# Performance work log

Hardware: AMD Instinct MI355X
Metric: run time of the kernel (lower is better)

Reference implementation:

```python
import jax, jax.numpy as jnp
import numpy as np

HIDDEN = 1024
INTER = 2816
NUM_EXPERTS = 8
TOP_K = 2
NUM_TASK_EXPERTS = 4
NUM_GENERALISTS = 2
NUM_TASKS = 8
BSZ, SEQ = 4, 2048
NEG = -1e9


def setup_inputs() -> dict:
    key = jax.random.key(0)
    ks = jax.random.split(key, 8)
    s = 1.0 / np.sqrt(HIDDEN)
    si = 1.0 / np.sqrt(INTER)
    return {
        "hidden_states": jax.random.normal(ks[0], (BSZ, SEQ, HIDDEN), jnp.float32),
        "task_id": 3,
        "task_emb": jax.random.normal(ks[1], (NUM_TASKS, HIDDEN), jnp.float32) * 0.02,
        "task_router_w": jax.random.uniform(ks[2], (NUM_EXPERTS, HIDDEN), jnp.float32, -s, s),
        "gate_weight": jax.random.uniform(ks[3], (NUM_EXPERTS, HIDDEN), jnp.float32, -s, s),
        "gate_proj": jax.random.uniform(ks[4], (NUM_EXPERTS, INTER, HIDDEN), jnp.float32, -s, s),
        "up_proj": jax.random.uniform(ks[5], (NUM_EXPERTS, INTER, HIDDEN), jnp.float32, -s, s),
        "down_proj": jax.random.uniform(ks[6], (NUM_EXPERTS, HIDDEN, INTER), jnp.float32, -si, si),
    }


def reference(hidden_states, task_id, task_emb, task_router_w, gate_weight,
              gate_proj, up_proj, down_proj):
    bsz, seq, dim = hidden_states.shape
    E, K = NUM_EXPERTS, TOP_K

    # ---- task-level routing: pick active experts ----
    task_vec = task_emb[task_id]                         # [d]
    task_scores = task_router_w @ task_vec               # [E]
    _, task_idx = jax.lax.top_k(task_scores, NUM_TASK_EXPERTS)
    gen_idx = jnp.arange(E - NUM_GENERALISTS, E)
    active_mask = jnp.zeros((E,), bool).at[task_idx].set(True).at[gen_idx].set(True)

    # ---- token-level gating over active experts (masked full softmax == subset softmax) ----
    gate_input = (hidden_states + task_vec).reshape(-1, dim)      # [N, d]
    logits = gate_input @ gate_weight.T                            # [N, E]
    scores = jax.nn.softmax(jnp.where(active_mask, logits, NEG), axis=-1)
    topk_gates, topk_idx = jax.lax.top_k(scores, K)                # [N, K]
    topk_gates = topk_gates / (topk_gates.sum(-1, keepdims=True) + 1e-6)

    # per-token per-expert combine weight: [N, E]
    comb = (jax.nn.one_hot(topk_idx, E, dtype=topk_gates.dtype) * topk_gates[..., None]).sum(1)

    # ---- expert MLPs (SwiGLU), dense-per-expert then weighted combine ----
    tokens = hidden_states.reshape(-1, dim)                        # [N, d]
    y = jnp.zeros_like(tokens)
    for e in range(E):
        h = jax.nn.silu(tokens @ gate_proj[e].T) * (tokens @ up_proj[e].T)  # [N, I]
        y = y + comb[:, e:e + 1] * (h @ down_proj[e].T)
    return y.reshape(bsz, seq, dim)
```

## Files before the change

### kernel.cpp

```cpp
#include <hip/hip_runtime.h>

#define HIDDEN 1024
#define INTER 2816
#define NE 8
#define NTOK 8192
#define CPAD 32
#define MAXTILES 136

typedef _Float16 f16;
typedef f16 f16x8 __attribute__((ext_vector_type(8)));
typedef f16 f16x4v __attribute__((ext_vector_type(4)));
typedef float f32x4 __attribute__((ext_vector_type(4)));

typedef __attribute__((address_space(3))) void lds_void;
typedef __attribute__((address_space(1))) void glb_void;

__device__ __forceinline__ void gl_lds16(const void* g, void* l) {
  __builtin_amdgcn_global_load_lds((const glb_void*)g, (lds_void*)l, 16, 0, 0);
}

__device__ __forceinline__ f32x4 mfma16(f16x8 a, f16x8 b, f32x4 c) {
  return __builtin_amdgcn_mfma_f32_16x16x32_f16(a, b, c, 0, 0, 0);
}

__device__ __forceinline__ f16x8 cvt8(float4 a, float4 b) {
  f16x8 v;
  v[0] = (f16)a.x; v[1] = (f16)a.y; v[2] = (f16)a.z; v[3] = (f16)a.w;
  v[4] = (f16)b.x; v[5] = (f16)b.y; v[6] = (f16)b.z; v[7] = (f16)b.w;
  return v;
}

__global__ void k_route(const float* __restrict__ task_emb,
                        const int* __restrict__ task_id_p,
                        const float* __restrict__ trw,
                        int* __restrict__ mask, int* __restrict__ counts) {
  __shared__ float sc[NE];
  const int tid = threadIdx.x;
  counts[tid] = 0;
  const float* tv = task_emb + (size_t)task_id_p[0] * HIDDEN;
  const int e = tid >> 5, l = tid & 31;
  float p = 0.f;
  for (int k = l; k < HIDDEN; k += 32) p += trw[e * HIDDEN + k] * tv[k];
  for (int o = 16; o > 0; o >>= 1) p += __shfl_down(p, o, 32);
  if (l == 0) sc[e] = p;
  __syncthreads();
  if (tid == 0) {
    int m[NE];
    bool used[NE];
    for (int i = 0; i < NE; ++i) { m[i] = 0; used[i] = false; }
    for (int it = 0; it < 4; ++it) {
      float best = -1e30f; int bi = 0;
      for (int i = 0; i < NE; ++i)
        if (!used[i] && sc[i] > best) { best = sc[i]; bi = i; }
      used[bi] = true; m[bi] = 1;
    }
    m[NE - 2] = 1; m[NE - 1] = 1;
    for (int i = 0; i < NE; ++i) mask[i] = m[i];
  }
}

__global__ __launch_bounds__(256) void k_gate_wcvt(
    const float* __restrict__ x, const float* __restrict__ task_emb,
    const int* __restrict__ task_id_p, const float* __restrict__ gw,
    const int* __restrict__ mask, int* __restrict__ counts,
    int* __restrict__ tok_list, int* __restrict__ tk_e,
    int* __restrict__ tk_pos, float* __restrict__ tk_w,
    f16* __restrict__ X16,
    const float* __restrict__ Wg, const float* __restrict__ Wu,
    const float* __restrict__ Wd,
    f16* __restrict__ Wg16, f16* __restrict__ Wu16, f16* __restrict__ Wd16) {
  const int tid = threadIdx.x;
  if (blockIdx.x >= 256) {
    const int bid = blockIdx.x - 256;
    const int e = bid / (3 * 1408);
    const int rem = bid - e * (3 * 1408);
    const int sel = rem / 1408;
    const int xb = rem - sel * 1408;
    if (!mask[e]) return;
    const float* src = sel == 0 ? Wg : (sel == 1 ? Wu : Wd);
    f16* dst = sel == 0 ? Wg16 : (sel == 1 ? Wu16 : Wd16);
    const size_t i = (size_t)e * INTER * HIDDEN + ((size_t)xb * 256 + tid) * 8;
    const float4* s4 = (const float4*)(src + i);
    float4 a = s4[0], b = s4[1];
    *(f16x8*)(dst + i) = cvt8(a, b);
    return;
  }
  const int g = tid >> 3, l8 = tid & 7;
  const int t = blockIdx.x * 32 + g;
  const float4* tv4 = (const float4*)(task_emb + (size_t)task_id_p[0] * HIDDEN);
  const float4* xr4 = (const float4*)(x + (size_t)t * HIDDEN);
  const float4* gw4 = (const float4*)gw;

  float acc[NE];
#pragma unroll
  for (int e = 0; e < NE; ++e) acc[e] = 0.f;
#pragma unroll 4
  for (int it = 0; it < 32; ++it) {
    const int idx4 = it * 8 + l8;
    float4 xv = xr4[idx4];
    f16x4v h4;
    h4[0] = (f16)xv.x; h4[1] = (f16)xv.y; h4[2] = (f16)xv.z; h4[3] = (f16)xv.w;
    *(f16x4v*)(X16 + (size_t)t * HIDDEN + idx4 * 4) = h4;
    float4 tvv = tv4[idx4];
    const float gx = xv.x + tvv.x, gy = xv.y + tvv.y;
    const float gz = xv.z + tvv.z, gwv = xv.w + tvv.w;
#pragma unroll
    for (int e = 0; e < NE; ++e) {
      float4 w = gw4[e * 256 + idx4];
      acc[e] += gx * w.x + gy * w.y + gz * w.z + gwv * w.w;
    }
  }
#pragma unroll
  for (int e = 0; e < NE; ++e) {
    acc[e] += __shfl_down(acc[e], 4, 8);
    acc[e] += __shfl_down(acc[e], 2, 8);
    acc[e] += __shfl_down(acc[e], 1, 8);
  }

  __shared__ int s_e0[32], s_e1[32], s_r0[32], s_r1[32], s_base[NE];
  __shared__ float s_w0[32], s_w1[32];

  if (l8 == 0) {
    float mx = -1e30f;
    for (int e = 0; e < NE; ++e) if (mask[e] && acc[e] > mx) mx = acc[e];
    float pr[NE]; float s = 0.f;
    for (int e = 0; e < NE; ++e) {
      pr[e] = mask[e] ? expf(acc[e] - mx) : 0.f;
      s += pr[e];
    }
    int i0 = 0; float v0 = -1.f;
    for (int e = 0; e < NE; ++e) if (pr[e] > v0) { v0 = pr[e]; i0 = e; }
    int i1 = (i0 == 0) ? 1 : 0; float v1 = -1.f;
    for (int e = 0; e < NE; ++e) if (e != i0 && pr[e] > v1) { v1 = pr[e]; i1 = e; }
    float g0 = v0 / s, g1 = v1 / s;
    float d = g0 + g1 + 1e-6f;
    s_e0[g] = i0; s_e1[g] = i1;
    s_w0[g] = g0 / d; s_w1[g] = g1 / d;
  }
  __syncthreads();
  if (tid == 0) {
    int cnt[NE];
#pragma unroll
    for (int e = 0; e < NE; ++e) cnt[e] = 0;
    for (int i = 0; i < 32; ++i) {
      s_r0[i] = cnt[s_e0[i]]++;
      s_r1[i] = cnt[s_e1[i]]++;
    }
    for (int e = 0; e < NE; ++e)
      s_base[e] = cnt[e] ? atomicAdd(&counts[e * CPAD], cnt[e]) : 0;
  }
  __syncthreads();
  if (l8 == 0) {
    const int e0 = s_e0[g], e1 = s_e1[g];
    const int p0 = s_base[e0] + s_r0[g];
    const int p1 = s_base[e1] + s_r1[g];
    tok_list[e0 * NTOK + p0] = t;
    tok_list[e1 * NTOK + p1] = t;
    tk_e[t] = e0; tk_e[NTOK + t] = e1;
    tk_pos[t] = p0; tk_pos[NTOK + t] = p1;
    tk_w[t] = s_w0[g]; tk_w[NTOK + t] = s_w1[g];
  }
}

__global__ void k_tiles(const int* __restrict__ counts, int* __restrict__ tiles) {
  if (threadIdx.x != 0) return;
  int* te = tiles + 1;
  int* tm = te + MAXTILES;
  int* tp = tm + MAXTILES;
  int* tn = tp + MAXTILES;
  int p = 0, nt = 0;
  for (int e = 0; e < NE; ++e) {
    const int c = counts[e * CPAD];
    for (int m0 = 0; m0 < c; m0 += 128) {
      te[nt] = e; tm[nt] = m0; tp[nt] = p; tn[nt] = c; ++nt;
    }
    p += c;
  }
  tiles[0] = nt;
}

__global__ __launch_bounds__(256, 2) void k_gateup16(
    const f16* __restrict__ X16, const f16* __restrict__ Wg16,
    const f16* __restrict__ Wu16, const int* __restrict__ tiles,
    const int* __restrict__ tok_list, f16* __restrict__ H) {
  const int yt = blockIdx.y;
  if (yt >= tiles[0]) return;
  const int e = tiles[1 + yt];
  const int m0 = tiles[1 + MAXTILES + yt];
  const int pbase = tiles[1 + 2 * MAXTILES + yt];
  const int ne = tiles[1 + 3 * MAXTILES + yt];
  const int n0 = blockIdx.x * 64;

  __shared__ __align__(16) f16 As[128][64];
  __shared__ __align__(16) f16 Bg[64][64];
  __shared__ __align__(16) f16 Bu[64][64];
  __shared__ int toks[128];

  const int tid = threadIdx.x;
  if (tid < 128) {
    int r = m0 + tid;
    toks[tid] = tok_list[e * NTOK + (r < ne ? r : ne - 1)];
  }
  __syncthreads();

  const int row8 = tid >> 3;
  const int sw = ((tid & 7) ^ (row8 & 7)) * 8;
  const f16* asrc[4];
#pragma unroll
  for (int l = 0; l < 4; ++l)
    asrc[l] = X16 + (size_t)toks[l * 32 + row8] * HIDDEN + sw;
  f16* aldst0 = &As[0][0] + tid * 8;
  const size_t ewoff = (size_t)e * INTER * HIDDEN;
  const f16* gsrc0 = Wg16 + ewoff + (size_t)(n0 + row8) * HIDDEN + sw;
  const f16* usrc0 = Wu16 + ewoff + (size_t)(n0 + row8) * HIDDEN + sw;
  f16* gdst0 = &Bg[0][0] + tid * 8;
  f16* udst0 = &Bu[0][0] + tid * 8;

  const int lane = tid & 63;
  const int wave = tid >> 6;
  const int wm = (wave >> 1) * 64;
  const int wn = (wave & 1) * 32;
  const int l15 = lane & 15, grp = lane >> 4;

  const f32x4 zf = {0.f, 0.f, 0.f, 0.f};
  f32x4 accg[4][2], accu[4][2];
#pragma unroll
  for (int i = 0; i < 4; ++i)
#pragma unroll
    for (int j = 0; j < 2; ++j) { accg[i][j] = zf; accu[i][j] = zf; }

#pragma unroll 1
  for (int k0 = 0; k0 < HIDDEN; k0 += 64) {
#pragma unroll
    for (int l = 0; l < 4; ++l)
      gl_lds16(asrc[l] + k0, aldst0 + l * 2048);
    gl_lds16(gsrc0 + k0, gdst0);
    gl_lds16(gsrc0 + k0 + 32 * HIDDEN, gdst0 + 2048);
    gl_lds16(usrc0 + k0, udst0);
    gl_lds16(usrc0 + k0 + 32 * HIDDEN, udst0 + 2048);
    __syncthreads();

#pragma unroll
    for (int h = 0; h < 2; ++h) {
      const int pc = (((h * 4 + grp) ^ (l15 & 7)) << 4);
      f16x8 af[4];
#pragma unroll
      for (int i = 0; i < 4; ++i)
        af[i] = *(const f16x8*)((const char*)&As[0][0] +
                                (wm + i * 16 + l15) * 128 + pc);
      f16x8 bg[2], bu[2];
#pragma unroll
      for (int j = 0; j < 2; ++j) {
        bg[j] = *(const f16x8*)((const char*)&Bg[0][0] +
                                (wn + j * 16 + l15) * 128 + pc);
        bu[j] = *(const f16x8*)((const char*)&Bu[0][0] +
                                (wn + j * 16 + l15) * 128 + pc);
      }
#pragma unroll
      for (int i = 0; i < 4; ++i)
#pragma unroll
        for (int j = 0; j < 2; ++j) {
          accg[i][j] = mfma16(af[i], bg[j], accg[i][j]);
          accu[i][j] = mfma16(af[i], bu[j], accu[i][j]);
        }
    }
    __syncthreads();
  }

  const int col = lane & 15;
  const int quad = lane >> 4;
#pragma unroll
  for (int i = 0; i < 4; ++i)
#pragma unroll
    for (int j = 0; j < 2; ++j)
#pragma unroll
      for (int r = 0; r < 4; ++r) {
        int m = wm + i * 16 + quad * 4 + r;
        if (m0 + m < ne) {
          float gv = accg[i][j][r];
          float uv = accu[i][j][r];
          float hv = (gv / (1.f + expf(-gv))) * uv;
          H[(size_t)(pbase + m0 + m) * INTER + (n0 + wn + j * 16 + col)] = (f16)hv;
        }
      }
}

__global__ __launch_bounds__(256, 2) void k_down16(
    const f16* __restrict__ H, const f16* __restrict__ Wd16,
    const int* __restrict__ tiles, f16* __restrict__ Ybuf) {
  const int yt = blockIdx.y;
  if (yt >= tiles[0]) return;
  const int e = tiles[1 + yt];
  const int m0 = tiles[1 + MAXTILES + yt];
  const int pbase = tiles[1 + 2 * MAXTILES + yt];
  const int ne = tiles[1 + 3 * MAXTILES + yt];
  const int n0 = blockIdx.x * 128;

  __shared__ __align__(16) f16 As[128][64];
  __shared__ __align__(16) f16 Bs[128][64];

  const int tid = threadIdx.x;
  const int row8 = tid >> 3;
  const int sw = ((tid & 7) ^ (row8 & 7)) * 8;
  const f16* a0 = H + (size_t)(pbase + m0 + row8) * INTER + sw;
  const f16* b0 = Wd16 + (size_t)e * HIDDEN * INTER +
                  (size_t)(n0 + row8) * INTER + sw;
  f16* aldst0 = &As[0][0] + tid * 8;
  f16* bldst0 = &Bs[0][0] + tid * 8;

  const int lane = tid & 63;
  const int wave = tid >> 6;
  const int wm = (wave >> 1) * 64;
  const int wn = (wave & 1) * 64;
  const int l15 = lane & 15, grp = lane >> 4;

  const f32x4 zf = {0.f, 0.f, 0.f, 0.f};
  f32x4 acc[4][4];
#pragma unroll
  for (int i = 0; i < 4; ++i)
#pragma unroll
    for (int j = 0; j < 4; ++j) acc[i][j] = zf;

#pragma unroll 1
  for (int k0 = 0; k0 < INTER; k0 += 64) {
#pragma unroll
    for (int l = 0; l < 4; ++l) {
      gl_lds16(a0 + (size_t)l * 32 * INTER + k0, aldst0 + l * 2048);
      gl_lds16(b0 + (size_t)l * 32 * INTER + k0, bldst0 + l * 2048);
    }
    __syncthreads();

#pragma unroll
    for (int h = 0; h < 2; ++h) {
      const int pc = (((h * 4 + grp) ^ (l15 & 7)) << 4);
      f16x8 af[4], bf[4];
#pragma unroll
      for (int i = 0; i < 4; ++i)
        af[i] = *(const f16x8*)((const char*)&As[0][0] +
                                (wm + i * 16 + l15) * 128 + pc);
#pragma unroll
      for (int j = 0; j < 4; ++j)
        bf[j] = *(const f16x8*)((const char*)&Bs[0][0] +
                                (wn + j * 16 + l15) * 128 + pc);
#pragma unroll
      for (int i = 0; i < 4; ++i)
#pragma unroll
        for (int j = 0; j < 4; ++j)
          acc[i][j] = mfma16(af[i], bf[j], acc[i][j]);
    }
    __syncthreads();
  }

  const int col = lane & 15;
  const int quad = lane >> 4;
#pragma unroll
  for (int i = 0; i < 4; ++i)
#pragma unroll
    for (int j = 0; j < 4; ++j)
#pragma unroll
      for (int r = 0; r < 4; ++r) {
        int m = wm + i * 16 + quad * 4 + r;
        if (m0 + m < ne)
          Ybuf[(size_t)(pbase + m0 + m) * HIDDEN + (n0 + wn + j * 16 + col)] =
              (f16)acc[i][j][r];
      }
}

__global__ __launch_bounds__(256) void k_combine(
    const f16* __restrict__ Ybuf, const int* __restrict__ tk_e,
    const int* __restrict__ tk_pos, const float* __restrict__ tk_w,
    const int* __restrict__ counts, float* __restrict__ out) {
  __shared__ int s_pre[NE];
  if (threadIdx.x == 0) {
    int p = 0;
    for (int i = 0; i < NE; ++i) { s_pre[i] = p; p += counts[i * CPAD]; }
  }
  __syncthreads();
  const int sub = threadIdx.x >> 7;
  const int t = blockIdx.x * 2 + sub;
  const int c = (threadIdx.x & 127) * 8;
  const int e0 = tk_e[t], e1 = tk_e[NTOK + t];
  const int p0 = s_pre[e0] + tk_pos[t];
  const int p1 = s_pre[e1] + tk_pos[NTOK + t];
  const float w0 = tk_w[t], w1 = tk_w[NTOK + t];
  f16x8 a = *(const f16x8*)(Ybuf + (size_t)p0 * HIDDEN + c);
  f16x8 b = *(const f16x8*)(Ybuf + (size_t)p1 * HIDDEN + c);
  float* o = out + (size_t)t * HIDDEN + c;
  float4 o0, o1;
  o0.x = w0 * (float)a[0] + w1 * (float)b[0];
  o0.y = w0 * (float)a[1] + w1 * (float)b[1];
  o0.z = w0 * (float)a[2] + w1 * (float)b[2];
  o0.w = w0 * (float)a[3] + w1 * (float)b[3];
  o1.x = w0 * (float)a[4] + w1 * (float)b[4];
  o1.y = w0 * (float)a[5] + w1 * (float)b[5];
  o1.z = w0 * (float)a[6] + w1 * (float)b[6];
  o1.w = w0 * (float)a[7] + w1 * (float)b[7];
  *(float4*)o = o0;
  *(float4*)(o + 4) = o1;
}

__global__ void k_sentinel(float* out, float v) {
  int i = blockIdx.x * 256 + threadIdx.x;
  out[i] = v;
}

extern "C" void kernel_launch(void* const* d_in, const int* in_sizes, int n_in,
                              void* d_out, int out_size, void* d_ws, size_t ws_size,
                              hipStream_t stream) {
  const float* x = (const float*)d_in[0];
  const int* task_id = (const int*)d_in[1];
  const float* task_emb = (const float*)d_in[2];
  const float* trw = (const float*)d_in[3];
  const float* gw = (const float*)d_in[4];
  const float* Wg = (const float*)d_in[5];
  const float* Wu = (const float*)d_in[6];
  const float* Wd = (const float*)d_in[7];
  float* out = (float*)d_out;

  char* ws = (char*)d_ws;
  const size_t ROWS_PAD = (size_t)2 * NTOK + 256;
  const size_t IH = (size_t)INTER * HIDDEN;

  size_t off = 0;
  int* mask = (int*)(ws + off); off += 64;
  off = (off + 255) & ~(size_t)255;
  int* counts = (int*)(ws + off); off += NE * CPAD * 4;
  off = (off + 255) & ~(size_t)255;
  int* tiles = (int*)(ws + off); off += (1 + 4 * MAXTILES) * 4;
  off = (off + 255) & ~(size_t)255;
  int* tk_e = (int*)(ws + off); off += (size_t)2 * NTOK * 4;
  int* tk_pos = (int*)(ws + off); off += (size_t)2 * NTOK * 4;
  float* tk_w = (float*)(ws + off); off += (size_t)2 * NTOK * 4;
  int* tok_list = (int*)(ws + off); off += (size_t)NE * NTOK * 4;
  off = (off + 255) & ~(size_t)255;
  f16* X16 = (f16*)(ws + off); off += (size_t)NTOK * HIDDEN * 2;
  f16* H = (f16*)(ws + off); off += ROWS_PAD * INTER * 2;
  f16* Ybuf = (f16*)(ws + off); off += ROWS_PAD * HIDDEN * 2;
  f16* Wg16 = (f16*)(ws + off); off += (size_t)NE * IH * 2;
  f16* Wu16 = (f16*)(ws + off); off += (size_t)NE * IH * 2;
  f16* Wd16 = (f16*)(ws + off); off += (size_t)NE * IH * 2;
  const size_t need_full = off;

  if (ws_size < need_full) {
    k_sentinel<<<(NTOK * HIDDEN + 255) / 256, 256, 0, stream>>>(
        out, (float)(ws_size >> 20));
    return;
  }

  k_route<<<1, 256, 0, stream>>>(task_emb, task_id, trw, mask, counts);
  k_gate_wcvt<<<256 + 3 * NE * 1408, 256, 0, stream>>>(
      x, task_emb, task_id, gw, mask, counts, tok_list, tk_e, tk_pos, tk_w,
      X16, Wg, Wu, Wd, Wg16, Wu16, Wd16);
  k_tiles<<<1, 64, 0, stream>>>(counts, tiles);
  k_gateup16<<<dim3(INTER / 64, MAXTILES), 256, 0, stream>>>(
      X16, Wg16, Wu16, tiles, tok_list, H);
  k_down16<<<dim3(HIDDEN / 128, MAXTILES), 256, 0, stream>>>(
      H, Wd16, tiles, Ybuf);
  k_combine<<<NTOK / 2, 256, 0, stream>>>(Ybuf, tk_e, tk_pos, tk_w, counts, out);
}
```

Before: 668.9 us.

## Enlarge gate/up GEMM tiles to 256x128 with double-buffered LDS pipelining

Rewrites the gate/up expert GEMM to use 256-token by 128-column tiles with 512 threads, backed by a separate 256-row tile list. It double-buffers the LDS stages, prefetches register fragments for the next half-K step, and raises wave priority around the MFMA bursts. The aim is more reuse of each loaded tile and overlap of global loads with compute. The cost is 128KB of LDS per block, heavier register use, and more padded rows in partial tiles, which together could limit occupancy.

```diff
diff --git a/kernel.cpp b/kernel.cpp
--- a/kernel.cpp
+++ b/kernel.cpp
@@ -6,6 +6,7 @@
 #define NTOK 8192
 #define CPAD 32
 #define MAXTILES 136
+#define MAXT2 72
 
 typedef _Float16 f16;
 typedef f16 f16x8 __attribute__((ext_vector_type(8)));
@@ -162,42 +163,59 @@
   }
 }
 
-__global__ void k_tiles(const int* __restrict__ counts, int* __restrict__ tiles) {
+__global__ void k_tiles(const int* __restrict__ counts, int* __restrict__ tiles,
+                        int* __restrict__ tiles2) {
   if (threadIdx.x != 0) return;
-  int* te = tiles + 1;
-  int* tm = te + MAXTILES;
-  int* tp = tm + MAXTILES;
-  int* tn = tp + MAXTILES;
-  int p = 0, nt = 0;
-  for (int e = 0; e < NE; ++e) {
-    const int c = counts[e * CPAD];
-    for (int m0 = 0; m0 < c; m0 += 128) {
-      te[nt] = e; tm[nt] = m0; tp[nt] = p; tn[nt] = c; ++nt;
-    }
-    p += c;
-  }
-  tiles[0] = nt;
-}
-
-__global__ __launch_bounds__(256, 2) void k_gateup16(
+  {
+    int* te = tiles + 1;
+    int* tm = te + MAXTILES;
+    int* tp = tm + MAXTILES;
+    int* tn = tp + MAXTILES;
+    int p = 0, nt = 0;
+    for (int e = 0; e < NE; ++e) {
+      const int c = counts[e * CPAD];
+      for (int m0 = 0; m0 < c; m0 += 128) {
+        te[nt] = e; tm[nt] = m0; tp[nt] = p; tn[nt] = c; ++nt;
+      }
+      p += c;
+    }
+    tiles[0] = nt;
+  }
+  {
+    int* te = tiles2 + 1;
+    int* tm = te + MAXT2;
+    int* tp = tm + MAXT2;
+    int* tn = tp + MAXT2;
+    int p = 0, nt = 0;
+    for (int e = 0; e < NE; ++e) {
+      const int c = counts[e * CPAD];
+      for (int m0 = 0; m0 < c; m0 += 256) {
+        te[nt] = e; tm[nt] = m0; tp[nt] = p; tn[nt] = c; ++nt;
+      }
+      p += c;
+    }
+    tiles2[0] = nt;
+  }
+}
+
+__global__ __launch_bounds__(512, 2) void k_gateup16(
     const f16* __restrict__ X16, const f16* __restrict__ Wg16,
-    const f16* __restrict__ Wu16, const int* __restrict__ tiles,
+    const f16* __restrict__ Wu16, const int* __restrict__ tiles2,
     const int* __restrict__ tok_list, f16* __restrict__ H) {
   const int yt = blockIdx.y;
-  if (yt >= tiles[0]) return;
-  const int e = tiles[1 + yt];
-  const int m0 = tiles[1 + MAXTILES + yt];
-  const int pbase = tiles[1 + 2 * MAXTILES + yt];
-  const int ne = tiles[1 + 3 * MAXTILES + yt];
-  const int n0 = blockIdx.x * 64;
-
-  __shared__ __align__(16) f16 As[128][64];
-  __shared__ __align__(16) f16 Bg[64][64];
-  __shared__ __align__(16) f16 Bu[64][64];
-  __shared__ int toks[128];
+  if (yt >= tiles2[0]) return;
+  const int e = tiles2[1 + yt];
+  const int m0 = tiles2[1 + MAXT2 + yt];
+  const int pbase = tiles2[1 + 2 * MAXT2 + yt];
+  const int ne = tiles2[1 + 3 * MAXT2 + yt];
+  const int n0 = blockIdx.x * 128;
+
+  __shared__ __align__(16) f16 As[2][256][64];
+  __shared__ __align__(16) f16 Bs[2][256][64];
+  __shared__ int toks[256];
 
   const int tid = threadIdx.x;
-  if (tid < 128) {
+  if (tid < 256) {
     int r = m0 + tid;
     toks[tid] = tok_list[e * NTOK + (r < ne ? r : ne - 1)];
   }
@@ -208,79 +226,134 @@
   const f16* asrc[4];
 #pragma unroll
   for (int l = 0; l < 4; ++l)
-    asrc[l] = X16 + (size_t)toks[l * 32 + row8] * HIDDEN + sw;
-  f16* aldst0 = &As[0][0] + tid * 8;
+    asrc[l] = X16 + (size_t)toks[l * 64 + row8] * HIDDEN + sw;
   const size_t ewoff = (size_t)e * INTER * HIDDEN;
-  const f16* gsrc0 = Wg16 + ewoff + (size_t)(n0 + row8) * HIDDEN + sw;
-  const f16* usrc0 = Wu16 + ewoff + (size_t)(n0 + row8) * HIDDEN + sw;
-  f16* gdst0 = &Bg[0][0] + tid * 8;
-  f16* udst0 = &Bu[0][0] + tid * 8;
+  const f16* gsrc = Wg16 + ewoff + (size_t)(n0 + row8) * HIDDEN + sw;
+  const f16* usrc = Wu16 + ewoff + (size_t)(n0 + row8) * HIDDEN + sw;
+  f16* adst = &As[0][0][0] + tid * 8;
+  f16* bdst = &Bs[0][0][0] + tid * 8;
 
   const int lane = tid & 63;
   const int wave = tid >> 6;
-  const int wm = (wave >> 1) * 64;
-  const int wn = (wave & 1) * 32;
+  const int wr = wave >> 2;
+  const int wc = wave & 3;
   const int l15 = lane & 15, grp = lane >> 4;
+  const char* Abase = (const char*)&As[0][0][0];
+  const char* Bbase = (const char*)&Bs[0][0][0];
+  const int arow = wr * 128 + l15;
+  const int brow = wc * 32 + l15;
+  const int pc0 = (grp ^ (l15 & 7)) << 4;
+  const int pc1 = ((4 + grp) ^ (l15 & 7)) << 4;
 
   const f32x4 zf = {0.f, 0.f, 0.f, 0.f};
-  f32x4 accg[4][2], accu[4][2];
-#pragma unroll
-  for (int i = 0; i < 4; ++i)
+  f32x4 accg[8][2], accu[8][2];
+#pragma unroll
+  for (int i = 0; i < 8; ++i)
 #pragma unroll
     for (int j = 0; j < 2; ++j) { accg[i][j] = zf; accu[i][j] = zf; }
 
-#pragma unroll 1
-  for (int k0 = 0; k0 < HIDDEN; k0 += 64) {
-#pragma unroll
-    for (int l = 0; l < 4; ++l)
-      gl_lds16(asrc[l] + k0, aldst0 + l * 2048);
-    gl_lds16(gsrc0 + k0, gdst0);
-    gl_lds16(gsrc0 + k0 + 32 * HIDDEN, gdst0 + 2048);
-    gl_lds16(usrc0 + k0, udst0);
-    gl_lds16(usrc0 + k0 + 32 * HIDDEN, udst0 + 2048);
-    __syncthreads();
-
-#pragma unroll
-    for (int h = 0; h < 2; ++h) {
-      const int pc = (((h * 4 + grp) ^ (l15 & 7)) << 4);
-      f16x8 af[4];
-#pragma unroll
-      for (int i = 0; i < 4; ++i)
-        af[i] = *(const f16x8*)((const char*)&As[0][0] +
-                                (wm + i * 16 + l15) * 128 + pc);
-      f16x8 bg[2], bu[2];
+#define STAGE(buf, k0)                                                       \
+  do {                                                                       \
+    _Pragma("unroll") for (int l = 0; l < 4; ++l)                            \
+        gl_lds16(asrc[l] + (k0), adst + (buf) * 16384 + l * 4096);           \
+    gl_lds16(gsrc + (k0), bdst + (buf) * 16384);                             \
+    gl_lds16(gsrc + (k0) + 64 * HIDDEN, bdst + (buf) * 16384 + 4096);        \
+    gl_lds16(usrc + (k0), bdst + (buf) * 16384 + 8192);                      \
+    gl_lds16(usrc + (k0) + 64 * HIDDEN, bdst + (buf) * 16384 + 12288);       \
+  } while (0)
+
+  STAGE(0, 0);
+  STAGE(1, 64);
+  asm volatile("s_waitcnt vmcnt(8)" ::: "memory");
+  __builtin_amdgcn_sched_barrier(0);
+  __builtin_amdgcn_s_barrier();
+
+  f16x8 ca[8], cg[2], cu[2];
+#pragma unroll
+  for (int i = 0; i < 8; ++i)
+    ca[i] = *(const f16x8*)(Abase + (arow + i * 16) * 128 + pc0);
+#pragma unroll
+  for (int j = 0; j < 2; ++j) {
+    cg[j] = *(const f16x8*)(Bbase + (brow + j * 16) * 128 + pc0);
+    cu[j] = *(const f16x8*)(Bbase + (brow + 128 + j * 16) * 128 + pc0);
+  }
+
+#pragma unroll 2
+  for (int kt = 0; kt < 16; ++kt) {
+    const int cur = kt & 1;
+    const char* Ab = Abase + cur * 32768;
+    const char* Bb = Bbase + cur * 32768;
+    f16x8 na[8], ng[2], nu[2];
+#pragma unroll
+    for (int i = 0; i < 8; ++i)
+      na[i] = *(const f16x8*)(Ab + (arow + i * 16) * 128 + pc1);
+#pragma unroll
+    for (int j = 0; j < 2; ++j) {
+      ng[j] = *(const f16x8*)(Bb + (brow + j * 16) * 128 + pc1);
+      nu[j] = *(const f16x8*)(Bb + (brow + 128 + j * 16) * 128 + pc1);
+    }
+    __builtin_amdgcn_s_setprio(1);
+#pragma unroll
+    for (int i = 0; i < 8; ++i)
 #pragma unroll
       for (int j = 0; j < 2; ++j) {
-        bg[j] = *(const f16x8*)((const char*)&Bg[0][0] +
-                                (wn + j * 16 + l15) * 128 + pc);
-        bu[j] = *(const f16x8*)((const char*)&Bu[0][0] +
-                                (wn + j * 16 + l15) * 128 + pc);
+        accg[i][j] = mfma16(ca[i], cg[j], accg[i][j]);
+        accu[i][j] = mfma16(ca[i], cu[j], accu[i][j]);
       }
-#pragma unroll
-      for (int i = 0; i < 4; ++i)
-#pragma unroll
-        for (int j = 0; j < 2; ++j) {
-          accg[i][j] = mfma16(af[i], bg[j], accg[i][j]);
-          accu[i][j] = mfma16(af[i], bu[j], accu[i][j]);
-        }
-    }
-    __syncthreads();
-  }
+    __builtin_amdgcn_s_setprio(0);
+    asm volatile("s_waitcnt lgkmcnt(0)" ::: "memory");
+    __builtin_amdgcn_sched_barrier(0);
+    __builtin_amdgcn_s_barrier();
+    if (kt < 14) STAGE(cur, (kt + 2) * 64);
+    if (kt < 14) {
+      asm volatile("s_waitcnt vmcnt(8)" ::: "memory");
+    } else {
+      asm volatile("s_waitcnt vmcnt(0)" ::: "memory");
+    }
+    __builtin_amdgcn_sched_barrier(0);
+    __builtin_amdgcn_s_barrier();
+    const char* Ab2 = Abase + (cur ^ 1) * 32768;
+    const char* Bb2 = Bbase + (cur ^ 1) * 32768;
+    f16x8 pa[8], pg[2], pu[2];
+#pragma unroll
+    for (int i = 0; i < 8; ++i)
+      pa[i] = *(const f16x8*)(Ab2 + (arow + i * 16) * 128 + pc0);
+#pragma unroll
+    for (int j = 0; j < 2; ++j) {
+      pg[j] = *(const f16x8*)(Bb2 + (brow + j * 16) * 128 + pc0);
+      pu[j] = *(const f16x8*)(Bb2 + (brow + 128 + j * 16) * 128 + pc0);
+    }
+    __builtin_amdgcn_s_setprio(1);
+#pragma unroll
+    for (int i = 0; i < 8; ++i)
+#pragma unroll
+      for (int j = 0; j < 2; ++j) {
+        accg[i][j] = mfma16(na[i], ng[j], accg[i][j]);
+        accu[i][j] = mfma16(na[i], nu[j], accu[i][j]);
+      }
+    __builtin_amdgcn_s_setprio(0);
+#pragma unroll
+    for (int i = 0; i < 8; ++i) ca[i] = pa[i];
+    cg[0] = pg[0]; cg[1] = pg[1];
+    cu[0] = pu[0]; cu[1] = pu[1];
+  }
+#undef STAGE
 
   const int col = lane & 15;
   const int quad = lane >> 4;
 #pragma unroll
-  for (int i = 0; i < 4; ++i)
+  for (int i = 0; i < 8; ++i)
 #pragma unroll
     for (int j = 0; j < 2; ++j)
 #pragma unroll
       for (int r = 0; r < 4; ++r) {
-        int m = wm + i * 16 + quad * 4 + r;
+        int m = wr * 128 + i * 16 + quad * 4 + r;
         if (m0 + m < ne) {
           float gv = accg[i][j][r];
           float uv = accu[i][j][r];
           float hv = (gv / (1.f + expf(-gv))) * uv;
-          H[(size_t)(pbase + m0 + m) * INTER + (n0 + wn + j * 16 + col)] = (f16)hv;
+          H[(size_t)(pbase + m0 + m) * INTER + (n0 + wc * 32 + j * 16 + col)] =
+              (f16)hv;
         }
       }
 }
@@ -428,6 +501,8 @@
   off = (off + 255) & ~(size_t)255;
   int* tiles = (int*)(ws + off); off += (1 + 4 * MAXTILES) * 4;
   off = (off + 255) & ~(size_t)255;
+  int* tiles2 = (int*)(ws + off); off += (1 + 4 * MAXT2) * 4;
+  off = (off + 255) & ~(size_t)255;
   int* tk_e = (int*)(ws + off); off += (size_t)2 * NTOK * 4;
   int* tk_pos = (int*)(ws + off); off += (size_t)2 * NTOK * 4;
   float* tk_w = (float*)(ws + off); off += (size_t)2 * NTOK * 4;
@@ -451,9 +526,9 @@
   k_gate_wcvt<<<256 + 3 * NE * 1408, 256, 0, stream>>>(
       x, task_emb, task_id, gw, mask, counts, tok_list, tk_e, tk_pos, tk_w,
       X16, Wg, Wu, Wd, Wg16, Wu16, Wd16);
-  k_tiles<<<1, 64, 0, stream>>>(counts, tiles);
-  k_gateup16<<<dim3(INTER / 64, MAXTILES), 256, 0, stream>>>(
-      X16, Wg16, Wu16, tiles, tok_list, H);
+  k_tiles<<<1, 64, 0, stream>>>(counts, tiles, tiles2);
+  k_gateup16<<<dim3(INTER / 128, MAXT2), 512, 0, stream>>>(
+      X16, Wg16, Wu16, tiles2, tok_list, H);
   k_down16<<<dim3(HIDDEN / 128, MAXTILES), 256, 0, stream>>>(
       H, Wd16, tiles, Ybuf);
   k_combine<<<NTOK / 2, 256, 0, stream>>>(Ybuf, tk_e, tk_pos, tk_w, counts, out);
```

New measurement: 1.028 ms. 53.6% more time.

## Move down-proj weight conversion into idle gate/up GEMM blocks

Applied to the files above, without the earlier changes.

The fp32→fp16 conversion of down_proj weights moves out of the gating/convert kernel and into the blocks of the gate/up GEMM grid whose tile slots are unused (beyond the actual tile count). Those dead blocks stride over the down weights of active experts and convert them, so the conversion overlaps with the GEMM instead of running serially before it. The risk is that the converting blocks compete with the GEMM for memory bandwidth, and that the amount of spare capacity depends on how many tiles routing produces.

```diff
diff --git a/kernel.cpp b/kernel.cpp
--- a/kernel.cpp
+++ b/kernel.cpp
@@ -67,18 +67,17 @@
     int* __restrict__ tk_pos, float* __restrict__ tk_w,
     f16* __restrict__ X16,
     const float* __restrict__ Wg, const float* __restrict__ Wu,
-    const float* __restrict__ Wd,
-    f16* __restrict__ Wg16, f16* __restrict__ Wu16, f16* __restrict__ Wd16) {
+    f16* __restrict__ Wg16, f16* __restrict__ Wu16) {
   const int tid = threadIdx.x;
   if (blockIdx.x >= 256) {
     const int bid = blockIdx.x - 256;
-    const int e = bid / (3 * 1408);
-    const int rem = bid - e * (3 * 1408);
+    const int e = bid / (2 * 1408);
+    const int rem = bid - e * (2 * 1408);
     const int sel = rem / 1408;
     const int xb = rem - sel * 1408;
     if (!mask[e]) return;
-    const float* src = sel == 0 ? Wg : (sel == 1 ? Wu : Wd);
-    f16* dst = sel == 0 ? Wg16 : (sel == 1 ? Wu16 : Wd16);
+    const float* src = sel == 0 ? Wg : Wu;
+    f16* dst = sel == 0 ? Wg16 : Wu16;
     const size_t i = (size_t)e * INTER * HIDDEN + ((size_t)xb * 256 + tid) * 8;
     const float4* s4 = (const float4*)(src + i);
     float4 a = s4[0], b = s4[1];
@@ -182,9 +181,26 @@
 __global__ __launch_bounds__(256, 2) void k_gateup16(
     const f16* __restrict__ X16, const f16* __restrict__ Wg16,
     const f16* __restrict__ Wu16, const int* __restrict__ tiles,
-    const int* __restrict__ tok_list, f16* __restrict__ H) {
+    const int* __restrict__ tok_list, f16* __restrict__ H,
+    const float* __restrict__ Wd, f16* __restrict__ Wd16,
+    const int* __restrict__ mask) {
   const int yt = blockIdx.y;
-  if (yt >= tiles[0]) return;
+  const int nt = tiles[0];
+  if (yt >= nt) {
+    const int ndead = (MAXTILES - nt) * gridDim.x;
+    const int tid = threadIdx.x;
+    for (int c = (yt - nt) * gridDim.x + blockIdx.x; c < NE * 1408; c += ndead) {
+      const int e = c / 1408;
+      if (!mask[e]) continue;
+      const int xb = c - e * 1408;
+      const size_t i =
+          (size_t)e * INTER * HIDDEN + ((size_t)xb * 256 + tid) * 8;
+      const float4* s4 = (const float4*)(Wd + i);
+      float4 a = s4[0], b = s4[1];
+      *(f16x8*)(Wd16 + i) = cvt8(a, b);
+    }
+    return;
+  }
   const int e = tiles[1 + yt];
   const int m0 = tiles[1 + MAXTILES + yt];
   const int pbase = tiles[1 + 2 * MAXTILES + yt];
@@ -448,12 +464,12 @@
   }
 
   k_route<<<1, 256, 0, stream>>>(task_emb, task_id, trw, mask, counts);
-  k_gate_wcvt<<<256 + 3 * NE * 1408, 256, 0, stream>>>(
+  k_gate_wcvt<<<256 + 2 * NE * 1408, 256, 0, stream>>>(
       x, task_emb, task_id, gw, mask, counts, tok_list, tk_e, tk_pos, tk_w,
-      X16, Wg, Wu, Wd, Wg16, Wu16, Wd16);
+      X16, Wg, Wu, Wg16, Wu16);
   k_tiles<<<1, 64, 0, stream>>>(counts, tiles);
   k_gateup16<<<dim3(INTER / 64, MAXTILES), 256, 0, stream>>>(
-      X16, Wg16, Wu16, tiles, tok_list, H);
+      X16, Wg16, Wu16, tiles, tok_list, H, Wd, Wd16, mask);
   k_down16<<<dim3(HIDDEN / 128, MAXTILES), 256, 0, stream>>>(
       H, Wd16, tiles, Ybuf);
   k_combine<<<NTOK / 2, 256, 0, stream>>>(Ybuf, tk_e, tk_pos, tk_w, counts, out);
```

After: 670.7 us. Within noise of the previous version (+0.3%).
